# Kernel optimization log

Hardware: AMD Instinct MI355X
Metric: run time of the kernel (lower is better)

## Reference

```python
import jax, jax.numpy as jnp
import numpy as np

N, F, U, H = 4096, 512, 64, 8
EDGE_PROB = 0.01
NEG_MASK = -10e9  # matches keras-gat masking constant
LRELU_SLOPE = 0.2


def setup_inputs() -> dict:
    key = jax.random.key(0)
    kX, kA, kI, kW, kS, kN, kB = jax.random.split(key, 7)
    X = jax.random.normal(kX, (1, N, F), dtype=jnp.float32)
    # sparse binary adjacency with self loops (layer expects preprocessed self-loops)
    A = (jax.random.uniform(kA, (N, N)) < EDGE_PROB).astype(jnp.float32)
    A = jnp.maximum(A, jnp.eye(N, dtype=jnp.float32))
    out_indices = jax.random.randint(kI, (1, 128), 0, N).astype(jnp.int64)
    scale_w = 1.0 / np.sqrt(F)
    scale_a = 1.0 / np.sqrt(U)
    W = jax.random.normal(kW, (H, F, U), dtype=jnp.float32) * scale_w
    a_self = jax.random.normal(kS, (H, U), dtype=jnp.float32) * scale_a
    a_neigh = jax.random.normal(kN, (H, U), dtype=jnp.float32) * scale_a
    bias = jax.random.normal(kB, (H, U), dtype=jnp.float32) * 0.1
    return {"X": X, "out_indices": out_indices, "A": A, "W": W,
            "a_self": a_self, "a_neigh": a_neigh, "bias": bias}


def reference(X, out_indices, A, W, a_self, a_neigh, bias):
    x = X[0]  # [N, F] (batch dim of 1)
    # per-head linear transform: [H, N, U]
    h = jnp.einsum('nf,hfu->hnu', x, W)
    # additive attention logits: f_self[i] + f_neigh[j]
    f_self = jnp.einsum('hnu,hu->hn', h, a_self)    # [H, N]
    f_neigh = jnp.einsum('hnu,hu->hn', h, a_neigh)  # [H, N]
    scores = f_self[:, :, None] + f_neigh[:, None, :]  # [H, N, N]
    scores = jax.nn.leaky_relu(scores, negative_slope=LRELU_SLOPE)
    # mask non-edges (standard, non-saliency path): dense += -10e9 * (1 - A)
    scores = scores + NEG_MASK * (1.0 - A)[None, :, :]
    attn = jax.nn.softmax(scores, axis=-1)  # [H, N, N]
    # weighted aggregation + bias
    out = jnp.einsum('hnm,hmu->hnu', attn, h) + bias[:, None, :]  # [H, N, U]
    # concat heads: [N, H*U], then activation (relu)
    out = jnp.transpose(out, (1, 0, 2)).reshape(N, H * U)
    out = jax.nn.relu(out)
    return out[None, :, :]  # [1, N, H*U]; final_layer=False -> all nodes
```

## Files before the change

### kernel.cpp

```cpp
#include <hip/hip_runtime.h>
#include <hip/hip_bf16.h>

#define N_NODES 4096
#define F_DIM   512
#define U_DIM   64
#define H_HEADS 8
#define C_DIM   512
#define LRELU_S 0.2f
#define MAXE    128
#define GEMM_BLOCKS 512

typedef __attribute__((ext_vector_type(8))) short bf16x8;
typedef __attribute__((ext_vector_type(4))) float f32x4;

__device__ inline unsigned short f2bf(float f) {
  union { float f; unsigned u; } v; v.f = f;
  unsigned r = v.u + 0x7FFFu + ((v.u >> 16) & 1u);
  return (unsigned short)(r >> 16);
}
__device__ inline float bf2f(unsigned short b) {
  union { unsigned u; float f; } v; v.u = ((unsigned)b) << 16;
  return v.f;
}

__global__ __launch_bounds__(256) void front_kernel(
    const float* __restrict__ X, const float* __restrict__ W,
    const float* __restrict__ A, const float* __restrict__ a_self,
    const float* __restrict__ a_neigh, unsigned short* __restrict__ hb,
    float* __restrict__ fs, float* __restrict__ fn, int* __restrict__ deg,
    unsigned short* __restrict__ nbr) {
  __shared__ unsigned short As[64][72];
  __shared__ unsigned short Bs[64][72];
  __shared__ int wsum[4];

  const int t    = threadIdx.x;
  const int lane = t & 63;
  const int w    = t >> 6;

  if ((int)blockIdx.x < GEMM_BLOCKS) {
    const int mblk = blockIdx.x & 63;
    const int head = blockIdx.x >> 6;
    const int m0   = mblk * 64;
    const float* Wh = W + (size_t)head * F_DIM * U_DIM;

    const int wr = w >> 1, wc = w & 1;
    const int arow = t >> 2;
    const int akc  = (t & 3) * 16;
    const int bu   = t & 63;
    const int bjc  = (t >> 6) * 16;

    f32x4 acc[2][2] = {};

    for (int k0 = 0; k0 < F_DIM; k0 += 64) {
      {
        const float* src = X + (size_t)(m0 + arow) * F_DIM + k0 + akc;
        float4 f0 = ((const float4*)src)[0];
        float4 f1 = ((const float4*)src)[1];
        float4 f2 = ((const float4*)src)[2];
        float4 f3 = ((const float4*)src)[3];
        bf16x8 u0 = {(short)f2bf(f0.x), (short)f2bf(f0.y), (short)f2bf(f0.z),
                     (short)f2bf(f0.w), (short)f2bf(f1.x), (short)f2bf(f1.y),
                     (short)f2bf(f1.z), (short)f2bf(f1.w)};
        bf16x8 u1 = {(short)f2bf(f2.x), (short)f2bf(f2.y), (short)f2bf(f2.z),
                     (short)f2bf(f2.w), (short)f2bf(f3.x), (short)f2bf(f3.y),
                     (short)f2bf(f3.z), (short)f2bf(f3.w)};
        *(bf16x8*)&As[arow][akc]     = u0;
        *(bf16x8*)&As[arow][akc + 8] = u1;
      }
      {
        float bv[16];
#pragma unroll
        for (int j = 0; j < 16; ++j)
          bv[j] = Wh[(size_t)(k0 + bjc + j) * U_DIM + bu];
        bf16x8 w0 = {(short)f2bf(bv[0]), (short)f2bf(bv[1]), (short)f2bf(bv[2]),
                     (short)f2bf(bv[3]), (short)f2bf(bv[4]), (short)f2bf(bv[5]),
                     (short)f2bf(bv[6]), (short)f2bf(bv[7])};
        bf16x8 w1 = {(short)f2bf(bv[8]),  (short)f2bf(bv[9]),
                     (short)f2bf(bv[10]), (short)f2bf(bv[11]),
                     (short)f2bf(bv[12]), (short)f2bf(bv[13]),
                     (short)f2bf(bv[14]), (short)f2bf(bv[15])};
        *(bf16x8*)&Bs[bu][bjc]     = w0;
        *(bf16x8*)&Bs[bu][bjc + 8] = w1;
      }
      __syncthreads();

      const int r  = lane & 15;
      const int ko = (lane >> 4) * 8;
#pragma unroll
      for (int kk = 0; kk < 2; ++kk) {
        bf16x8 af0 = *(const bf16x8*)&As[wr * 32 + r][kk * 32 + ko];
        bf16x8 af1 = *(const bf16x8*)&As[wr * 32 + 16 + r][kk * 32 + ko];
        bf16x8 bf0 = *(const bf16x8*)&Bs[wc * 32 + r][kk * 32 + ko];
        bf16x8 bf1 = *(const bf16x8*)&Bs[wc * 32 + 16 + r][kk * 32 + ko];
        acc[0][0] = __builtin_amdgcn_mfma_f32_16x16x32_bf16(af0, bf0, acc[0][0], 0, 0, 0);
        acc[0][1] = __builtin_amdgcn_mfma_f32_16x16x32_bf16(af0, bf1, acc[0][1], 0, 0, 0);
        acc[1][0] = __builtin_amdgcn_mfma_f32_16x16x32_bf16(af1, bf0, acc[1][0], 0, 0, 0);
        acc[1][1] = __builtin_amdgcn_mfma_f32_16x16x32_bf16(af1, bf1, acc[1][1], 0, 0, 0);
      }
      __syncthreads();
    }

#pragma unroll
    for (int mi = 0; mi < 2; ++mi) {
#pragma unroll
      for (int ni = 0; ni < 2; ++ni) {
        const int rb = wr * 32 + mi * 16 + (lane >> 4) * 4;
        const int cl = wc * 32 + ni * 16 + (lane & 15);
#pragma unroll
        for (int reg = 0; reg < 4; ++reg) {
          unsigned short hv = f2bf(acc[mi][ni][reg]);
          hb[(size_t)(m0 + rb + reg) * C_DIM + head * U_DIM + cl] = hv;
          As[rb + reg][cl] = hv;
        }
      }
    }
    __syncthreads();
    if (t < 128) {
      const int r = t & 63;
      const float* avec = (t >= 64) ? a_neigh + head * U_DIM
                                    : a_self + head * U_DIM;
      float s = 0.f;
#pragma unroll
      for (int u = 0; u < 64; ++u) s += bf2f(As[r][u]) * avec[u];
      float* dst = (t >= 64) ? fn : fs;
      dst[head * N_NODES + m0 + r] = s;
    }
  } else {
    const int i = (int)blockIdx.x - GEMM_BLOCKS;
    const float* Arow = A + (size_t)i * N_NODES;
    const int base = t * 16;
    float av[16];
#pragma unroll
    for (int q = 0; q < 4; ++q) {
      float4 x = *(const float4*)(Arow + base + q * 4);
      av[q * 4 + 0] = x.x;
      av[q * 4 + 1] = x.y;
      av[q * 4 + 2] = x.z;
      av[q * 4 + 3] = x.w;
    }
    int c = 0;
#pragma unroll
    for (int q = 0; q < 16; ++q) c += (av[q] != 0.0f) ? 1 : 0;

    int psum = c;
#pragma unroll
    for (int off = 1; off < 64; off <<= 1) {
      int v = __shfl_up(psum, off);
      if (lane >= off) psum += v;
    }
    if (lane == 63) wsum[w] = psum;
    __syncthreads();
    int woff = 0;
#pragma unroll
    for (int k = 0; k < 4; ++k)
      if (k < w) woff += wsum[k];
    int E = wsum[0] + wsum[1] + wsum[2] + wsum[3];
    if (E > MAXE) E = MAXE;

    int pos = woff + psum - c;
#pragma unroll
    for (int q = 0; q < 16; ++q) {
      if (av[q] != 0.0f) {
        if (pos < MAXE) nbr[(size_t)i * MAXE + pos] = (unsigned short)(base + q);
        ++pos;
      }
    }
    if (t == 0) deg[i] = E;
  }
}

__global__ __launch_bounds__(256) void attn_kernel(
    const unsigned short* __restrict__ hb, const float* __restrict__ fs,
    const float* __restrict__ fn, const float* __restrict__ bias,
    const int* __restrict__ deg, const unsigned short* __restrict__ nbr,
    float* __restrict__ out) {
  __shared__ int   eidx[MAXE];
  __shared__ float p[H_HEADS][MAXE];

  const int i    = blockIdx.x;
  const int t    = threadIdx.x;
  const int lane = t & 63;
  const int w    = t >> 6;
  const int E    = deg[i];

  if (t < E) eidx[t] = (int)nbr[(size_t)i * MAXE + t];
  __syncthreads();

#pragma unroll
  for (int hh = 0; hh < 2; ++hh) {
    const int h = 2 * w + hh;
    const float fsi = fs[h * N_NODES + i];
    const float* fnh = fn + h * N_NODES;
    float lmax = -1e30f;
    for (int e = lane; e < E; e += 64) {
      float sc = fsi + fnh[eidx[e]];
      sc = (sc > 0.f) ? sc : LRELU_S * sc;
      p[h][e] = sc;
      lmax = fmaxf(lmax, sc);
    }
#pragma unroll
    for (int off = 32; off > 0; off >>= 1)
      lmax = fmaxf(lmax, __shfl_xor(lmax, off));
    float lsum = 0.f;
    for (int e = lane; e < E; e += 64) {
      float pe = __expf(p[h][e] - lmax);
      p[h][e] = pe;
      lsum += pe;
    }
#pragma unroll
    for (int off = 32; off > 0; off >>= 1) lsum += __shfl_xor(lsum, off);
    const float inv = 1.0f / lsum;
    for (int e = lane; e < E; e += 64) p[h][e] *= inv;
  }
  __syncthreads();

  const int cbase = w * 128 + 2 * lane;
  const int h = cbase >> 6;
  const float* ph = p[h];
  float acc0 = 0.f, acc1 = 0.f;
#pragma unroll 4
  for (int e = 0; e < E; ++e) {
    unsigned v = *(const unsigned*)(hb + (size_t)eidx[e] * C_DIM + cbase);
    float pe = ph[e];
    acc0 += pe * bf2f((unsigned short)(v & 0xFFFFu));
    acc1 += pe * bf2f((unsigned short)(v >> 16));
  }
  float2 bv = *(const float2*)(bias + cbase);
  out[(size_t)i * C_DIM + cbase]     = fmaxf(acc0 + bv.x, 0.f);
  out[(size_t)i * C_DIM + cbase + 1] = fmaxf(acc1 + bv.y, 0.f);
}

extern "C" void kernel_launch(void* const* d_in, const int* in_sizes, int n_in,
                              void* d_out, int out_size, void* d_ws,
                              size_t ws_size, hipStream_t stream) {
  const float* X       = (const float*)d_in[0];
  const float* A       = (const float*)d_in[2];
  const float* W       = (const float*)d_in[3];
  const float* a_self  = (const float*)d_in[4];
  const float* a_neigh = (const float*)d_in[5];
  const float* bias    = (const float*)d_in[6];
  float* out = (float*)d_out;

  unsigned short* hb = (unsigned short*)d_ws;
  float* fs = (float*)(hb + (size_t)N_NODES * C_DIM);
  float* fn = fs + (size_t)H_HEADS * N_NODES;
  int* deg  = (int*)(fn + (size_t)H_HEADS * N_NODES);
  unsigned short* nbr = (unsigned short*)(deg + N_NODES);

  front_kernel<<<GEMM_BLOCKS + N_NODES, 256, 0, stream>>>(
      X, W, A, a_self, a_neigh, hb, fs, fn, deg, nbr);

  attn_kernel<<<N_NODES, 256, 0, stream>>>(hb, fs, fn, bias, deg, nbr, out);
}
```

Baseline: 46.22 us.

## Use 128x128 GEMM tiles with register-side attention logits and two-node attention blocks

The projection GEMM moves to 128x128 tiles spanning two heads with a 32-wide K step and 16 MFMAs per wave per step. The self and neighbour logits are computed from the fp32 accumulators via shuffles instead of going through shared memory. The attention kernel processes two nodes per block with four heads per wave and 8-byte gathers, and defers softmax normalisation to the end, removing a barrier and a pass. Cutting the GEMM grid to 128 blocks may leave CUs idle during the GEMM phase.

```diff
diff --git a/kernel.cpp b/kernel.cpp
--- a/kernel.cpp
+++ b/kernel.cpp
@@ -8,7 +8,7 @@
 #define C_DIM   512
 #define LRELU_S 0.2f
 #define MAXE    128
-#define GEMM_BLOCKS 512
+#define GEMM_BLOCKS 128
 
 typedef __attribute__((ext_vector_type(8))) short bf16x8;
 typedef __attribute__((ext_vector_type(4))) float f32x4;
@@ -29,8 +29,8 @@
     const float* __restrict__ a_neigh, unsigned short* __restrict__ hb,
     float* __restrict__ fs, float* __restrict__ fn, int* __restrict__ deg,
     unsigned short* __restrict__ nbr) {
-  __shared__ unsigned short As[64][72];
-  __shared__ unsigned short Bs[64][72];
+  __shared__ unsigned short As[128][40];
+  __shared__ unsigned short Bs[128][40];
   __shared__ int wsum[4];
 
   const int t    = threadIdx.x;
@@ -38,22 +38,25 @@
   const int w    = t >> 6;
 
   if ((int)blockIdx.x < GEMM_BLOCKS) {
-    const int mblk = blockIdx.x & 63;
-    const int head = blockIdx.x >> 6;
-    const int m0   = mblk * 64;
-    const float* Wh = W + (size_t)head * F_DIM * U_DIM;
+    const int hp   = blockIdx.x & 3;
+    const int mblk = blockIdx.x >> 2;
+    const int m0   = mblk * 128;
+    const int n0   = hp * 128;
 
     const int wr = w >> 1, wc = w & 1;
-    const int arow = t >> 2;
-    const int akc  = (t & 3) * 16;
-    const int bu   = t & 63;
-    const int bjc  = (t >> 6) * 16;
-
-    f32x4 acc[2][2] = {};
-
-    for (int k0 = 0; k0 < F_DIM; k0 += 64) {
+
+    const int arow = t >> 1;
+    const int akq  = (t & 1) * 16;
+    const int bcl = t & 127;
+    const int bkq = (t >> 7) * 16;
+    const int bgc = n0 + bcl;
+    const float* wcol = W + ((size_t)(bgc >> 6) * F_DIM) * U_DIM + (bgc & 63);
+
+    f32x4 acc[4][4] = {};
+
+    for (int k0 = 0; k0 < F_DIM; k0 += 32) {
       {
-        const float* src = X + (size_t)(m0 + arow) * F_DIM + k0 + akc;
+        const float* src = X + (size_t)(m0 + arow) * F_DIM + k0 + akq;
         float4 f0 = ((const float4*)src)[0];
         float4 f1 = ((const float4*)src)[1];
         float4 f2 = ((const float4*)src)[2];
@@ -64,14 +67,14 @@
         bf16x8 u1 = {(short)f2bf(f2.x), (short)f2bf(f2.y), (short)f2bf(f2.z),
                      (short)f2bf(f2.w), (short)f2bf(f3.x), (short)f2bf(f3.y),
                      (short)f2bf(f3.z), (short)f2bf(f3.w)};
-        *(bf16x8*)&As[arow][akc]     = u0;
-        *(bf16x8*)&As[arow][akc + 8] = u1;
+        *(bf16x8*)&As[arow][akq]     = u0;
+        *(bf16x8*)&As[arow][akq + 8] = u1;
       }
       {
         float bv[16];
 #pragma unroll
         for (int j = 0; j < 16; ++j)
-          bv[j] = Wh[(size_t)(k0 + bjc + j) * U_DIM + bu];
+          bv[j] = wcol[(size_t)(k0 + bkq + j) * U_DIM];
         bf16x8 w0 = {(short)f2bf(bv[0]), (short)f2bf(bv[1]), (short)f2bf(bv[2]),
                      (short)f2bf(bv[3]), (short)f2bf(bv[4]), (short)f2bf(bv[5]),
                      (short)f2bf(bv[6]), (short)f2bf(bv[7])};
@@ -79,51 +82,73 @@
                      (short)f2bf(bv[10]), (short)f2bf(bv[11]),
                      (short)f2bf(bv[12]), (short)f2bf(bv[13]),
                      (short)f2bf(bv[14]), (short)f2bf(bv[15])};
-        *(bf16x8*)&Bs[bu][bjc]     = w0;
-        *(bf16x8*)&Bs[bu][bjc + 8] = w1;
+        *(bf16x8*)&Bs[bcl][bkq]     = w0;
+        *(bf16x8*)&Bs[bcl][bkq + 8] = w1;
       }
       __syncthreads();
 
       const int r  = lane & 15;
       const int ko = (lane >> 4) * 8;
-#pragma unroll
-      for (int kk = 0; kk < 2; ++kk) {
-        bf16x8 af0 = *(const bf16x8*)&As[wr * 32 + r][kk * 32 + ko];
-        bf16x8 af1 = *(const bf16x8*)&As[wr * 32 + 16 + r][kk * 32 + ko];
-        bf16x8 bf0 = *(const bf16x8*)&Bs[wc * 32 + r][kk * 32 + ko];
-        bf16x8 bf1 = *(const bf16x8*)&Bs[wc * 32 + 16 + r][kk * 32 + ko];
-        acc[0][0] = __builtin_amdgcn_mfma_f32_16x16x32_bf16(af0, bf0, acc[0][0], 0, 0, 0);
-        acc[0][1] = __builtin_amdgcn_mfma_f32_16x16x32_bf16(af0, bf1, acc[0][1], 0, 0, 0);
-        acc[1][0] = __builtin_amdgcn_mfma_f32_16x16x32_bf16(af1, bf0, acc[1][0], 0, 0, 0);
-        acc[1][1] = __builtin_amdgcn_mfma_f32_16x16x32_bf16(af1, bf1, acc[1][1], 0, 0, 0);
-      }
+      bf16x8 af[4], bfr[4];
+#pragma unroll
+      for (int mi = 0; mi < 4; ++mi)
+        af[mi] = *(const bf16x8*)&As[wr * 64 + mi * 16 + r][ko];
+#pragma unroll
+      for (int ni = 0; ni < 4; ++ni)
+        bfr[ni] = *(const bf16x8*)&Bs[wc * 64 + ni * 16 + r][ko];
+#pragma unroll
+      for (int mi = 0; mi < 4; ++mi)
+#pragma unroll
+        for (int ni = 0; ni < 4; ++ni)
+          acc[mi][ni] = __builtin_amdgcn_mfma_f32_16x16x32_bf16(
+              af[mi], bfr[ni], acc[mi][ni], 0, 0, 0);
       __syncthreads();
     }
 
-#pragma unroll
-    for (int mi = 0; mi < 2; ++mi) {
-#pragma unroll
-      for (int ni = 0; ni < 2; ++ni) {
-        const int rb = wr * 32 + mi * 16 + (lane >> 4) * 4;
-        const int cl = wc * 32 + ni * 16 + (lane & 15);
+    const int head = hp * 2 + wc;
+#pragma unroll
+    for (int mi = 0; mi < 4; ++mi) {
+#pragma unroll
+      for (int ni = 0; ni < 4; ++ni) {
+        const int row = m0 + wr * 64 + mi * 16 + (lane >> 4) * 4;
+        const int col = n0 + wc * 64 + ni * 16 + (lane & 15);
+#pragma unroll
+        for (int reg = 0; reg < 4; ++reg)
+          hb[(size_t)(row + reg) * C_DIM + col] = f2bf(acc[mi][ni][reg]);
+      }
+    }
+
+    {
+      float asv[4], anv[4];
+#pragma unroll
+      for (int ni = 0; ni < 4; ++ni) {
+        const int u = wc * 64 + ni * 16 + (lane & 15) - wc * 64;
+        asv[ni] = a_self[head * U_DIM + ni * 16 + (lane & 15)];
+        anv[ni] = a_neigh[head * U_DIM + ni * 16 + (lane & 15)];
+        (void)u;
+      }
+#pragma unroll
+      for (int mi = 0; mi < 4; ++mi) {
 #pragma unroll
         for (int reg = 0; reg < 4; ++reg) {
-          unsigned short hv = f2bf(acc[mi][ni][reg]);
-          hb[(size_t)(m0 + rb + reg) * C_DIM + head * U_DIM + cl] = hv;
-          As[rb + reg][cl] = hv;
+          float ps = 0.f, pn = 0.f;
+#pragma unroll
+          for (int ni = 0; ni < 4; ++ni) {
+            ps += acc[mi][ni][reg] * asv[ni];
+            pn += acc[mi][ni][reg] * anv[ni];
+          }
+#pragma unroll
+          for (int off = 1; off < 16; off <<= 1) {
+            ps += __shfl_xor(ps, off);
+            pn += __shfl_xor(pn, off);
+          }
+          if ((lane & 15) == 0) {
+            const int row = m0 + wr * 64 + mi * 16 + (lane >> 4) * 4 + reg;
+            fs[head * N_NODES + row] = ps;
+            fn[head * N_NODES + row] = pn;
+          }
         }
       }
-    }
-    __syncthreads();
-    if (t < 128) {
-      const int r = t & 63;
-      const float* avec = (t >= 64) ? a_neigh + head * U_DIM
-                                    : a_self + head * U_DIM;
-      float s = 0.f;
-#pragma unroll
-      for (int u = 0; u < 64; ++u) s += bf2f(As[r][u]) * avec[u];
-      float* dst = (t >= 64) ? fn : fs;
-      dst[head * N_NODES + m0 + r] = s;
     }
   } else {
     const int i = (int)blockIdx.x - GEMM_BLOCKS;
@@ -174,28 +199,34 @@
     const float* __restrict__ fn, const float* __restrict__ bias,
     const int* __restrict__ deg, const unsigned short* __restrict__ nbr,
     float* __restrict__ out) {
-  __shared__ int   eidx[MAXE];
-  __shared__ float p[H_HEADS][MAXE];
-
-  const int i    = blockIdx.x;
+  __shared__ int   eidx[2][MAXE];
+  __shared__ float p[2][H_HEADS][MAXE];
+  __shared__ float sinv[2][H_HEADS];
+
   const int t    = threadIdx.x;
   const int lane = t & 63;
   const int w    = t >> 6;
+  const int nd   = w >> 1;
+  const int wn   = w & 1;
+  const int i    = blockIdx.x * 2 + nd;
   const int E    = deg[i];
 
-  if (t < E) eidx[t] = (int)nbr[(size_t)i * MAXE + t];
+  {
+    const int e = wn * 64 + lane;
+    if (e < E) eidx[nd][e] = (int)nbr[(size_t)i * MAXE + e];
+  }
   __syncthreads();
 
 #pragma unroll
-  for (int hh = 0; hh < 2; ++hh) {
-    const int h = 2 * w + hh;
+  for (int hh = 0; hh < 4; ++hh) {
+    const int h = wn * 4 + hh;
     const float fsi = fs[h * N_NODES + i];
     const float* fnh = fn + h * N_NODES;
     float lmax = -1e30f;
     for (int e = lane; e < E; e += 64) {
-      float sc = fsi + fnh[eidx[e]];
+      float sc = fsi + fnh[eidx[nd][e]];
       sc = (sc > 0.f) ? sc : LRELU_S * sc;
-      p[h][e] = sc;
+      p[nd][h][e] = sc;
       lmax = fmaxf(lmax, sc);
     }
 #pragma unroll
@@ -203,31 +234,37 @@
       lmax = fmaxf(lmax, __shfl_xor(lmax, off));
     float lsum = 0.f;
     for (int e = lane; e < E; e += 64) {
-      float pe = __expf(p[h][e] - lmax);
-      p[h][e] = pe;
+      float pe = __expf(p[nd][h][e] - lmax);
+      p[nd][h][e] = pe;
       lsum += pe;
     }
 #pragma unroll
     for (int off = 32; off > 0; off >>= 1) lsum += __shfl_xor(lsum, off);
-    const float inv = 1.0f / lsum;
-    for (int e = lane; e < E; e += 64) p[h][e] *= inv;
-  }
-  __syncthreads();
-
-  const int cbase = w * 128 + 2 * lane;
-  const int h = cbase >> 6;
-  const float* ph = p[h];
-  float acc0 = 0.f, acc1 = 0.f;
+    if (lane == 0) sinv[nd][h] = 1.0f / lsum;
+  }
+
+  const int cbase = wn * 256 + 4 * lane;
+  const int h = wn * 4 + (lane >> 4);
+  const float* ph = p[nd][h];
+  float a0 = 0.f, a1 = 0.f, a2 = 0.f, a3 = 0.f;
 #pragma unroll 4
   for (int e = 0; e < E; ++e) {
-    unsigned v = *(const unsigned*)(hb + (size_t)eidx[e] * C_DIM + cbase);
+    const unsigned short* hp_ = hb + (size_t)eidx[nd][e] * C_DIM + cbase;
+    uint2 v = *(const uint2*)hp_;
     float pe = ph[e];
-    acc0 += pe * bf2f((unsigned short)(v & 0xFFFFu));
-    acc1 += pe * bf2f((unsigned short)(v >> 16));
-  }
-  float2 bv = *(const float2*)(bias + cbase);
-  out[(size_t)i * C_DIM + cbase]     = fmaxf(acc0 + bv.x, 0.f);
-  out[(size_t)i * C_DIM + cbase + 1] = fmaxf(acc1 + bv.y, 0.f);
+    a0 += pe * bf2f((unsigned short)(v.x & 0xFFFFu));
+    a1 += pe * bf2f((unsigned short)(v.x >> 16));
+    a2 += pe * bf2f((unsigned short)(v.y & 0xFFFFu));
+    a3 += pe * bf2f((unsigned short)(v.y >> 16));
+  }
+  const float inv = sinv[nd][h];
+  float4 bv = *(const float4*)(bias + cbase);
+  float4 o;
+  o.x = fmaxf(a0 * inv + bv.x, 0.f);
+  o.y = fmaxf(a1 * inv + bv.y, 0.f);
+  o.z = fmaxf(a2 * inv + bv.z, 0.f);
+  o.w = fmaxf(a3 * inv + bv.w, 0.f);
+  *(float4*)(out + (size_t)i * C_DIM + cbase) = o;
 }
 
 extern "C" void kernel_launch(void* const* d_in, const int* in_sizes, int n_in,
@@ -250,5 +287,5 @@
   front_kernel<<<GEMM_BLOCKS + N_NODES, 256, 0, stream>>>(
       X, W, A, a_self, a_neigh, hb, fs, fn, deg, nbr);
 
-  attn_kernel<<<N_NODES, 256, 0, stream>>>(hb, fs, fn, bias, deg, nbr, out);
-}
+  attn_kernel<<<N_NODES / 2, 256, 0, stream>>>(hb, fs, fn, bias, deg, nbr, out);
+}
```

Measured after the change: 52.24 us. 13.0% more time.

## Process one node per wavefront with node-major attention logits and vectorized gathers

Applied to the files above, without the earlier changes.

Attention logits fs/fn are now stored node-major, so all eight heads for a node are fetched with two float4 loads. The attention kernel handles four nodes per block, one per wavefront, with no block barrier during the softmax. Softmax normalisation is deferred to the epilogue, and each lane gathers 8 bf16 values per neighbour with one 16-byte load. The adjacency scan now reads coalesced strided float4s, which changes the order of neighbours. The cost is fewer blocks and more registers per lane.

```diff
diff --git a/kernel.cpp b/kernel.cpp
--- a/kernel.cpp
+++ b/kernel.cpp
@@ -27,7 +27,7 @@
     const float* __restrict__ X, const float* __restrict__ W,
     const float* __restrict__ A, const float* __restrict__ a_self,
     const float* __restrict__ a_neigh, unsigned short* __restrict__ hb,
-    float* __restrict__ fs, float* __restrict__ fn, int* __restrict__ deg,
+    float* __restrict__ fsT, float* __restrict__ fnT, int* __restrict__ deg,
     unsigned short* __restrict__ nbr) {
   __shared__ unsigned short As[64][72];
   __shared__ unsigned short Bs[64][72];
@@ -122,25 +122,23 @@
       float s = 0.f;
 #pragma unroll
       for (int u = 0; u < 64; ++u) s += bf2f(As[r][u]) * avec[u];
-      float* dst = (t >= 64) ? fn : fs;
-      dst[head * N_NODES + m0 + r] = s;
+      float* dst = (t >= 64) ? fnT : fsT;
+      dst[(size_t)(m0 + r) * H_HEADS + head] = s;
     }
   } else {
     const int i = (int)blockIdx.x - GEMM_BLOCKS;
     const float* Arow = A + (size_t)i * N_NODES;
-    const int base = t * 16;
-    float av[16];
+    float av[4][4];
 #pragma unroll
     for (int q = 0; q < 4; ++q) {
-      float4 x = *(const float4*)(Arow + base + q * 4);
-      av[q * 4 + 0] = x.x;
-      av[q * 4 + 1] = x.y;
-      av[q * 4 + 2] = x.z;
-      av[q * 4 + 3] = x.w;
+      float4 x = *(const float4*)(Arow + 4 * t + q * 1024);
+      av[q][0] = x.x; av[q][1] = x.y; av[q][2] = x.z; av[q][3] = x.w;
     }
     int c = 0;
 #pragma unroll
-    for (int q = 0; q < 16; ++q) c += (av[q] != 0.0f) ? 1 : 0;
+    for (int q = 0; q < 4; ++q)
+#pragma unroll
+      for (int j = 0; j < 4; ++j) c += (av[q][j] != 0.0f) ? 1 : 0;
 
     int psum = c;
 #pragma unroll
@@ -159,10 +157,14 @@
 
     int pos = woff + psum - c;
 #pragma unroll
-    for (int q = 0; q < 16; ++q) {
-      if (av[q] != 0.0f) {
-        if (pos < MAXE) nbr[(size_t)i * MAXE + pos] = (unsigned short)(base + q);
-        ++pos;
+    for (int q = 0; q < 4; ++q) {
+#pragma unroll
+      for (int j = 0; j < 4; ++j) {
+        if (av[q][j] != 0.0f) {
+          if (pos < MAXE)
+            nbr[(size_t)i * MAXE + pos] = (unsigned short)(4 * t + q * 1024 + j);
+          ++pos;
+        }
       }
     }
     if (t == 0) deg[i] = E;
@@ -170,64 +172,101 @@
 }
 
 __global__ __launch_bounds__(256) void attn_kernel(
-    const unsigned short* __restrict__ hb, const float* __restrict__ fs,
-    const float* __restrict__ fn, const float* __restrict__ bias,
+    const unsigned short* __restrict__ hb, const float* __restrict__ fsT,
+    const float* __restrict__ fnT, const float* __restrict__ bias,
     const int* __restrict__ deg, const unsigned short* __restrict__ nbr,
     float* __restrict__ out) {
-  __shared__ int   eidx[MAXE];
-  __shared__ float p[H_HEADS][MAXE];
-
-  const int i    = blockIdx.x;
+  __shared__ int   eidx[4][MAXE];
+  __shared__ float p[4][MAXE][9];
+
   const int t    = threadIdx.x;
   const int lane = t & 63;
   const int w    = t >> 6;
+  const int i    = blockIdx.x * 4 + w;
   const int E    = deg[i];
 
-  if (t < E) eidx[t] = (int)nbr[(size_t)i * MAXE + t];
+  float fsv[8];
+  {
+    float4 a = *(const float4*)(fsT + (size_t)i * H_HEADS);
+    float4 b = *(const float4*)(fsT + (size_t)i * H_HEADS + 4);
+    fsv[0]=a.x; fsv[1]=a.y; fsv[2]=a.z; fsv[3]=a.w;
+    fsv[4]=b.x; fsv[5]=b.y; fsv[6]=b.z; fsv[7]=b.w;
+  }
+
+  float pmax[8];
+#pragma unroll
+  for (int h = 0; h < 8; ++h) pmax[h] = -1e30f;
+  for (int e = lane; e < E; e += 64) {
+    const int j = (int)nbr[(size_t)i * MAXE + e];
+    eidx[w][e] = j;
+    float4 a = *(const float4*)(fnT + (size_t)j * H_HEADS);
+    float4 b = *(const float4*)(fnT + (size_t)j * H_HEADS + 4);
+    float fnv[8] = {a.x, a.y, a.z, a.w, b.x, b.y, b.z, b.w};
+#pragma unroll
+    for (int h = 0; h < 8; ++h) {
+      float sc = fsv[h] + fnv[h];
+      sc = (sc > 0.f) ? sc : LRELU_S * sc;
+      p[w][e][h] = sc;
+      pmax[h] = fmaxf(pmax[h], sc);
+    }
+  }
+#pragma unroll
+  for (int h = 0; h < 8; ++h)
+#pragma unroll
+    for (int off = 32; off > 0; off >>= 1)
+      pmax[h] = fmaxf(pmax[h], __shfl_xor(pmax[h], off));
+
+  float psum[8] = {};
+  for (int e = lane; e < E; e += 64) {
+#pragma unroll
+    for (int h = 0; h < 8; ++h) {
+      float ex = __expf(p[w][e][h] - pmax[h]);
+      p[w][e][h] = ex;
+      psum[h] += ex;
+    }
+  }
+#pragma unroll
+  for (int h = 0; h < 8; ++h)
+#pragma unroll
+    for (int off = 32; off > 0; off >>= 1) psum[h] += __shfl_xor(psum[h], off);
+
   __syncthreads();
 
-#pragma unroll
-  for (int hh = 0; hh < 2; ++hh) {
-    const int h = 2 * w + hh;
-    const float fsi = fs[h * N_NODES + i];
-    const float* fnh = fn + h * N_NODES;
-    float lmax = -1e30f;
-    for (int e = lane; e < E; e += 64) {
-      float sc = fsi + fnh[eidx[e]];
-      sc = (sc > 0.f) ? sc : LRELU_S * sc;
-      p[h][e] = sc;
-      lmax = fmaxf(lmax, sc);
-    }
-#pragma unroll
-    for (int off = 32; off > 0; off >>= 1)
-      lmax = fmaxf(lmax, __shfl_xor(lmax, off));
-    float lsum = 0.f;
-    for (int e = lane; e < E; e += 64) {
-      float pe = __expf(p[h][e] - lmax);
-      p[h][e] = pe;
-      lsum += pe;
-    }
-#pragma unroll
-    for (int off = 32; off > 0; off >>= 1) lsum += __shfl_xor(lsum, off);
-    const float inv = 1.0f / lsum;
-    for (int e = lane; e < E; e += 64) p[h][e] *= inv;
-  }
-  __syncthreads();
-
-  const int cbase = w * 128 + 2 * lane;
-  const int h = cbase >> 6;
-  const float* ph = p[h];
-  float acc0 = 0.f, acc1 = 0.f;
-#pragma unroll 4
+  const int cbase = 8 * lane;
+  const int hl = lane >> 3;
+  float acc[8] = {};
   for (int e = 0; e < E; ++e) {
-    unsigned v = *(const unsigned*)(hb + (size_t)eidx[e] * C_DIM + cbase);
-    float pe = ph[e];
-    acc0 += pe * bf2f((unsigned short)(v & 0xFFFFu));
-    acc1 += pe * bf2f((unsigned short)(v >> 16));
-  }
-  float2 bv = *(const float2*)(bias + cbase);
-  out[(size_t)i * C_DIM + cbase]     = fmaxf(acc0 + bv.x, 0.f);
-  out[(size_t)i * C_DIM + cbase + 1] = fmaxf(acc1 + bv.y, 0.f);
+    const int j = eidx[w][e];
+    uint4 v = *(const uint4*)(hb + (size_t)j * C_DIM + cbase);
+    const float pe = p[w][e][hl];
+    acc[0] += pe * bf2f((unsigned short)(v.x & 0xFFFFu));
+    acc[1] += pe * bf2f((unsigned short)(v.x >> 16));
+    acc[2] += pe * bf2f((unsigned short)(v.y & 0xFFFFu));
+    acc[3] += pe * bf2f((unsigned short)(v.y >> 16));
+    acc[4] += pe * bf2f((unsigned short)(v.z & 0xFFFFu));
+    acc[5] += pe * bf2f((unsigned short)(v.z >> 16));
+    acc[6] += pe * bf2f((unsigned short)(v.w & 0xFFFFu));
+    acc[7] += pe * bf2f((unsigned short)(v.w >> 16));
+  }
+  float sum = psum[0];
+#pragma unroll
+  for (int h = 1; h < 8; ++h)
+    if (hl == h) sum = psum[h];
+  const float inv = 1.0f / sum;
+
+  float4 b0 = *(const float4*)(bias + cbase);
+  float4 b1 = *(const float4*)(bias + cbase + 4);
+  float4 o0, o1;
+  o0.x = fmaxf(acc[0] * inv + b0.x, 0.f);
+  o0.y = fmaxf(acc[1] * inv + b0.y, 0.f);
+  o0.z = fmaxf(acc[2] * inv + b0.z, 0.f);
+  o0.w = fmaxf(acc[3] * inv + b0.w, 0.f);
+  o1.x = fmaxf(acc[4] * inv + b1.x, 0.f);
+  o1.y = fmaxf(acc[5] * inv + b1.y, 0.f);
+  o1.z = fmaxf(acc[6] * inv + b1.z, 0.f);
+  o1.w = fmaxf(acc[7] * inv + b1.w, 0.f);
+  *(float4*)(out + (size_t)i * C_DIM + cbase)     = o0;
+  *(float4*)(out + (size_t)i * C_DIM + cbase + 4) = o1;
 }
 
 extern "C" void kernel_launch(void* const* d_in, const int* in_sizes, int n_in,
@@ -242,13 +281,13 @@
   float* out = (float*)d_out;
 
   unsigned short* hb = (unsigned short*)d_ws;
-  float* fs = (float*)(hb + (size_t)N_NODES * C_DIM);
-  float* fn = fs + (size_t)H_HEADS * N_NODES;
-  int* deg  = (int*)(fn + (size_t)H_HEADS * N_NODES);
+  float* fsT = (float*)(hb + (size_t)N_NODES * C_DIM);
+  float* fnT = fsT + (size_t)H_HEADS * N_NODES;
+  int* deg   = (int*)(fnT + (size_t)H_HEADS * N_NODES);
   unsigned short* nbr = (unsigned short*)(deg + N_NODES);
 
   front_kernel<<<GEMM_BLOCKS + N_NODES, 256, 0, stream>>>(
-      X, W, A, a_self, a_neigh, hb, fs, fn, deg, nbr);
-
-  attn_kernel<<<N_NODES, 256, 0, stream>>>(hb, fs, fn, bias, deg, nbr, out);
-}
+      X, W, A, a_self, a_neigh, hb, fsT, fnT, deg, nbr);
+
+  attn_kernel<<<N_NODES / 4, 256, 0, stream>>>(hb, fsT, fnT, bias, deg, nbr, out);
+}
```

Result: faster. 40.45 us (-12.5%).
